# Performance work log

Hardware: AMD Instinct MI355X
Metric: run time of the kernel (lower is better)

The kernel has to match this reference:

```python
import jax, jax.numpy as jnp
import numpy as np

C = 1024      # BIGNET_DIM
GROUPS = 256  # (1024*1024) / group_size(4096)

def _dequant(q4, norm):
    # q4: [GROUPS, 2048] ints in [0,256) packing two 4-bit codes per byte
    # (even positions = low nibble, odd positions = high nibble, as in
    #  block_quantize_4bit / block_dequantize_4bit). norm: [GROUPS, 1].
    lo = q4 % 16
    hi = q4 // 16
    q8 = jnp.stack([lo, hi], axis=-1).reshape(GROUPS, -1).astype(jnp.float32)  # [GROUPS, 4096]
    w = (q8 / 15.0 * 2.0 - 1.0) * norm
    return w.reshape(C, C)  # [out_features, in_features]

def setup_inputs() -> dict:
    key = jax.random.key(0)
    ks = jax.random.split(key, 6)
    x = jax.random.normal(ks[0], (16384, C), jnp.float32)
    wq4 = jax.random.randint(ks[1], (18, GROUPS, 2048), 0, 256, jnp.int32)
    wnorm = jax.random.uniform(ks[2], (18, GROUPS, 1), dtype=jnp.float32) * 0.05 + 1e-3
    lora_a = jax.random.normal(ks[3], (3, 32, C), jnp.float32) * 0.02
    lora_b = jax.random.normal(ks[4], (3, C, 32), jnp.float32) * 0.01
    ln_gamma = jnp.ones((5, C), jnp.float32)
    ln_beta = jnp.zeros((5, C), jnp.float32)
    return {"x": x, "wq4": wq4, "wnorm": wnorm, "lora_a": lora_a,
            "lora_b": lora_b, "ln_gamma": ln_gamma, "ln_beta": ln_beta}

def reference(x, wq4, wnorm, lora_a, lora_b, ln_gamma, ln_beta):
    def lin(h, i):
        # dequantize group-wise int4 weight, then linear (bias=False)
        return h @ _dequant(wq4[i], wnorm[i]).T

    def block(h, b, li):
        y = lin(h, 3 * b)
        if li is not None:  # QLoRALinear: parallel fp32 low-rank path
            y = y + (h @ lora_a[li].T) @ lora_b[li].T
        y = jax.nn.relu(y)
        y = jax.nn.relu(lin(y, 3 * b + 1))
        y = lin(y, 3 * b + 2)
        return y + h  # residual

    def ln(h, i):
        mu = jnp.mean(h, axis=-1, keepdims=True)
        var = jnp.mean((h - mu) ** 2, axis=-1, keepdims=True)
        return (h - mu) * jax.lax.rsqrt(var + 1e-5) * ln_gamma[i] + ln_beta[i]

    h = block(x, 0, 0); h = ln(h, 0)
    h = block(h, 1, None); h = ln(h, 1)
    h = block(h, 2, 1); h = ln(h, 2)
    h = block(h, 3, None); h = ln(h, 3)
    h = block(h, 4, 2); h = ln(h, 4)
    h = block(h, 5, None)
    return h
```

## Files before the change

kernel.cpp:

```cpp
#include <hip/hip_runtime.h>

typedef __bf16 bf16x8 __attribute__((ext_vector_type(8)));
typedef float f32x4 __attribute__((ext_vector_type(4)));

__device__ __forceinline__ unsigned short f32_to_bf16u(float f) {
  unsigned int u = __float_as_uint(f);
  u += 0x7fffu + ((u >> 16) & 1u);
  return (unsigned short)(u >> 16);
}
__device__ __forceinline__ float bf16u_to_f32(unsigned short s) {
  return __uint_as_float((unsigned int)s << 16);
}

__device__ __forceinline__ void async_copy16(const void* gptr, void* lptr) {
  __builtin_amdgcn_global_load_lds(
      (__attribute__((address_space(1))) void*)(unsigned long long)gptr,
      (__attribute__((address_space(3))) void*)(unsigned long long)lptr,
      16, 0, 0);
}

__global__ __launch_bounds__(256) void lora_ba_kernel(
    const float* __restrict__ lora_a, const float* __restrict__ lora_b,
    float* __restrict__ Wba)
{
  const int bid = blockIdx.x;
  const int li = bid >> 10;
  const int o = bid & 1023;
  const float* B = lora_b + li * 32768 + o * 32;
  const float* A = lora_a + li * 32768;
  const int c = threadIdx.x * 4;
  float4 acc = {0.f, 0.f, 0.f, 0.f};
#pragma unroll
  for (int r = 0; r < 32; r++) {
    const float br = B[r];
    const float4 a = *(const float4*)&A[r * 1024 + c];
    acc.x += br * a.x; acc.y += br * a.y; acc.z += br * a.z; acc.w += br * a.w;
  }
  *(float4*)&Wba[((size_t)li << 20) + o * 1024 + c] = acc;
}

__global__ __launch_bounds__(256) void dequant_kernel(
    const int* __restrict__ wq4, const float* __restrict__ wnorm,
    const float* __restrict__ Wba, unsigned short* __restrict__ Wd)
{
  const int gi = blockIdx.x * 256 + threadIdx.x;
  const int w = gi >> 19;
  const int rem = gi & 524287;
  const int q = wq4[gi];
  const float norm = wnorm[(w << 8) + (rem >> 11)];
  float w0 = ((float)(q & 15) * (2.0f / 15.0f) - 1.0f) * norm;
  float w1 = ((float)(q >> 4) * (2.0f / 15.0f) - 1.0f) * norm;
  const int p = rem << 1;
  const int li = (w == 0) ? 0 : (w == 6) ? 1 : (w == 12) ? 2 : -1;
  if (li >= 0) {
    const float2 ba = *(const float2*)&Wba[((size_t)li << 20) + p];
    w0 += ba.x;
    w1 += ba.y;
  }
  const unsigned int packed =
      ((unsigned int)f32_to_bf16u(w1) << 16) | (unsigned int)f32_to_bf16u(w0);
  *(unsigned int*)&Wd[((size_t)w << 20) + p] = packed;
}

__global__ __launch_bounds__(256) void cast_bf16_kernel(
    const float* __restrict__ x, unsigned short* __restrict__ o)
{
  const int i = blockIdx.x * 256 + threadIdx.x;
  const float4 v = ((const float4*)x)[i];
  ushort4 b;
  b.x = f32_to_bf16u(v.x);
  b.y = f32_to_bf16u(v.y);
  b.z = f32_to_bf16u(v.z);
  b.w = f32_to_bf16u(v.w);
  ((ushort4*)o)[i] = b;
}

template <int EPIL>
__global__ __launch_bounds__(512, 2) void gemm_bt(
    const unsigned short* __restrict__ A, const unsigned short* __restrict__ W,
    void* __restrict__ Out, const unsigned short* __restrict__ Res)
{
  constexpr int K = 1024;
  constexpr int N = 1024;
  __shared__ unsigned short lds[2][4][8192];

  const int tid = threadIdx.x;
  const int lane = tid & 63;
  const int wv = tid >> 6;
  const int wm = wv >> 2;
  const int wn = wv & 3;

  const int bid = blockIdx.x;
  const int l = (bid & 7) * 32 + (bid >> 3);
  const int m0 = (l >> 2) << 8;
  const int n0 = (l & 3) << 8;

  const int fr = lane & 15;
  const int q = lane >> 4;
  const int fr7 = fr & 7;

  const int srow = tid >> 3;
  const int schk = (tid & 7) ^ (srow & 7);
  const unsigned short* Asrc = A + (size_t)(m0 + srow) * K + schk * 8;
  const int nb0 = ((srow >> 5) << 6) + (srow & 31);
  const unsigned short* Wsrc = W + (size_t)(n0 + nb0) * K + schk * 8;

#define STAGE_A(mq, dbuf, kt)                                          \
  do {                                                                 \
    const unsigned short* s_ = Asrc + (size_t)(mq) * 64 * K + (kt);    \
    unsigned short* d_ = &lds[dbuf][(mq) ? 2 : 0][tid * 8];            \
    async_copy16(s_, d_);                                              \
    async_copy16(s_ + (size_t)128 * K, d_ + 4096);                     \
  } while (0)
#define STAGE_B(nq, dbuf, kt)                                          \
  do {                                                                 \
    const unsigned short* s_ = Wsrc + (size_t)(nq) * 32 * K + (kt);    \
    unsigned short* d_ = &lds[dbuf][(nq) ? 3 : 1][tid * 8];            \
    async_copy16(s_, d_);                                              \
    async_copy16(s_ + (size_t)128 * K, d_ + 4096);                     \
  } while (0)

  const int a_lane = (wm * 64 + fr) * 64;
  const int b_lane = (wn * 32 + fr) * 64;
  const int c0 = (q ^ fr7) << 3;
  const int c1 = ((4 + q) ^ fr7) << 3;

#define LDA4(dbuf, mq)                                                               \
  do {                                                                               \
    _Pragma("unroll") for (int ri = 0; ri < 4; ++ri) {                               \
      af[ri][0] = *(const bf16x8*)&lds[dbuf][(mq) ? 2 : 0][a_lane + ri * 1024 + c0]; \
      af[ri][1] = *(const bf16x8*)&lds[dbuf][(mq) ? 2 : 0][a_lane + ri * 1024 + c1]; \
    }                                                                                \
  } while (0)
#define LDB2(dst, dbuf, nq)                                                          \
  do {                                                                               \
    _Pragma("unroll") for (int rj = 0; rj < 2; ++rj) {                               \
      dst[rj][0] = *(const bf16x8*)&lds[dbuf][(nq) ? 3 : 1][b_lane + rj * 1024 + c0];\
      dst[rj][1] = *(const bf16x8*)&lds[dbuf][(nq) ? 3 : 1][b_lane + rj * 1024 + c1];\
    }                                                                                \
  } while (0)

#define MFMA16(ib, jb, BB)                                                    \
  do {                                                                        \
    _Pragma("unroll") for (int i2 = 0; i2 < 4; ++i2)                          \
    _Pragma("unroll") for (int j2 = 0; j2 < 2; ++j2) {                        \
      acc[(ib) + i2][(jb) + j2] = __builtin_amdgcn_mfma_f32_16x16x32_bf16(    \
          af[i2][0], BB[j2][0], acc[(ib) + i2][(jb) + j2], 0, 0, 0);          \
      acc[(ib) + i2][(jb) + j2] = __builtin_amdgcn_mfma_f32_16x16x32_bf16(    \
          af[i2][1], BB[j2][1], acc[(ib) + i2][(jb) + j2], 0, 0, 0);          \
    }                                                                         \
  } while (0)

#define PHASE_MFMA(ib, jb, BB)                           \
  do {                                                   \
    __builtin_amdgcn_s_barrier();                        \
    asm volatile("s_waitcnt lgkmcnt(0)" ::: "memory");   \
    __builtin_amdgcn_s_setprio(1);                       \
    MFMA16(ib, jb, BB);                                  \
    __builtin_amdgcn_s_setprio(0);                       \
    __builtin_amdgcn_s_barrier();                        \
  } while (0)
#define PHASE_MFMA_VM(ib, jb, BB)                        \
  do {                                                   \
    __builtin_amdgcn_s_barrier();                        \
    asm volatile("s_waitcnt lgkmcnt(0)" ::: "memory");   \
    __builtin_amdgcn_s_setprio(1);                       \
    MFMA16(ib, jb, BB);                                  \
    __builtin_amdgcn_s_setprio(0);                       \
    asm volatile("s_waitcnt vmcnt(6)" ::: "memory");     \
    __builtin_amdgcn_s_barrier();                        \
  } while (0)

  f32x4 acc[8][4];
#pragma unroll
  for (int a_ = 0; a_ < 8; ++a_)
#pragma unroll
    for (int b_ = 0; b_ < 4; ++b_) acc[a_][b_] = (f32x4){0.f, 0.f, 0.f, 0.f};

  bf16x8 af[4][2], bf0[2][2], bf1[2][2];

  STAGE_A(0, 0, 0);
  STAGE_B(0, 0, 0);
  STAGE_A(1, 0, 0);
  STAGE_B(1, 0, 0);
  STAGE_A(0, 1, 64);
  STAGE_B(0, 1, 64);
  STAGE_A(1, 1, 64);
  asm volatile("s_waitcnt vmcnt(6)" ::: "memory");
  __builtin_amdgcn_s_barrier();

  for (int it = 0; it < K / 128; ++it) {
    const int kb = it * 128;
    const int k2 = (kb + 128 < K) ? (kb + 128) : (K - 64);
    const int k3 = (kb + 192 < K) ? (kb + 192) : (K - 64);

    LDA4(0, 0);
    LDB2(bf0, 0, 0);
    STAGE_B(1, 1, kb + 64);
    PHASE_MFMA(0, 0, bf0);
    LDB2(bf1, 0, 1);
    STAGE_A(0, 0, k2);
    PHASE_MFMA(0, 2, bf1);
    LDA4(0, 1);
    STAGE_B(0, 0, k2);
    PHASE_MFMA(4, 0, bf0);
    STAGE_A(1, 0, k2);
    PHASE_MFMA_VM(4, 2, bf1);
    LDA4(1, 0);
    LDB2(bf0, 1, 0);
    STAGE_B(1, 0, k2);
    PHASE_MFMA(0, 0, bf0);
    LDB2(bf1, 1, 1);
    STAGE_A(0, 1, k3);
    PHASE_MFMA(0, 2, bf1);
    LDA4(1, 1);
    STAGE_B(0, 1, k3);
    PHASE_MFMA(4, 0, bf0);
    STAGE_A(1, 1, k3);
    PHASE_MFMA_VM(4, 2, bf1);
  }

  const int mb = m0 + wm * 128 + q * 4;
  const int nb = n0 + wn * 64 + fr;
#pragma unroll
  for (int i2 = 0; i2 < 8; ++i2) {
#pragma unroll
    for (int r = 0; r < 4; ++r) {
      const int m = mb + i2 * 16 + r;
#pragma unroll
      for (int j2 = 0; j2 < 4; ++j2) {
        const int n = nb + j2 * 16;
        float v = acc[i2][j2][r];
        if (EPIL == 0) {
          v = v > 0.f ? v : 0.f;
          ((unsigned short*)Out)[(size_t)m * N + n] = f32_to_bf16u(v);
        } else if (EPIL == 1) {
          v += bf16u_to_f32(Res[(size_t)m * N + n]);
          ((unsigned short*)Out)[(size_t)m * N + n] = f32_to_bf16u(v);
        } else {
          v += bf16u_to_f32(Res[(size_t)m * N + n]);
          ((float*)Out)[(size_t)m * N + n] = v;
        }
      }
    }
  }
#undef STAGE_A
#undef STAGE_B
#undef LDA4
#undef LDB2
#undef MFMA16
#undef PHASE_MFMA
#undef PHASE_MFMA_VM
}

__global__ __launch_bounds__(256) void ln_kernel(
    const unsigned short* __restrict__ s_bf, const float* __restrict__ gamma,
    const float* __restrict__ beta, unsigned short* __restrict__ h_bf)
{
  const int row = blockIdx.x;
  const int tid = threadIdx.x;
  const size_t base = (size_t)row * 1024;
  const ushort4 u = ((const ushort4*)(s_bf + base))[tid];
  float v0 = bf16u_to_f32(u.x), v1 = bf16u_to_f32(u.y);
  float v2 = bf16u_to_f32(u.z), v3 = bf16u_to_f32(u.w);
  float s = v0 + v1 + v2 + v3;
  float s2 = v0 * v0 + v1 * v1 + v2 * v2 + v3 * v3;
#pragma unroll
  for (int off = 32; off > 0; off >>= 1) {
    s += __shfl_down(s, off, 64);
    s2 += __shfl_down(s2, off, 64);
  }
  __shared__ float red[8];
  if ((tid & 63) == 0) {
    red[tid >> 6] = s;
    red[4 + (tid >> 6)] = s2;
  }
  __syncthreads();
  s = red[0] + red[1] + red[2] + red[3];
  s2 = red[4] + red[5] + red[6] + red[7];
  const float mu = s * (1.0f / 1024.0f);
  const float var = s2 * (1.0f / 1024.0f) - mu * mu;
  const float rs = rsqrtf(var + 1e-5f);
  const float4 g = ((const float4*)gamma)[tid];
  const float4 bb = ((const float4*)beta)[tid];
  ushort4 ob;
  ob.x = f32_to_bf16u((v0 - mu) * rs * g.x + bb.x);
  ob.y = f32_to_bf16u((v1 - mu) * rs * g.y + bb.y);
  ob.z = f32_to_bf16u((v2 - mu) * rs * g.z + bb.z);
  ob.w = f32_to_bf16u((v3 - mu) * rs * g.w + bb.w);
  ((ushort4*)(h_bf + base))[tid] = ob;
}

extern "C" void kernel_launch(void* const* d_in, const int* in_sizes, int n_in,
                              void* d_out, int out_size, void* d_ws, size_t ws_size,
                              hipStream_t stream)
{
  const float* x = (const float*)d_in[0];
  const int* wq4 = (const int*)d_in[1];
  const float* wnorm = (const float*)d_in[2];
  const float* lora_a = (const float*)d_in[3];
  const float* lora_b = (const float*)d_in[4];
  const float* ln_g = (const float*)d_in[5];
  const float* ln_b = (const float*)d_in[6];
  float* out = (float*)d_out;

  char* ws = (char*)d_ws;
  unsigned short* Wd   = (unsigned short*)(ws);
  unsigned short* x_bf = (unsigned short*)(ws + 37748736);
  unsigned short* t1   = (unsigned short*)(ws + 71303168);
  unsigned short* t2   = (unsigned short*)(ws + 104857600);
  unsigned short* s_bf = (unsigned short*)(ws + 138412032);
  unsigned short* h_bf = (unsigned short*)(ws + 171966464);
  float* Wba           = (float*)(ws + 138412032);

  lora_ba_kernel<<<3072, 256, 0, stream>>>(lora_a, lora_b, Wba);
  dequant_kernel<<<36864, 256, 0, stream>>>(wq4, wnorm, Wba, Wd);
  cast_bf16_kernel<<<16384, 256, 0, stream>>>(x, x_bf);

  const unsigned short* hb = x_bf;
  const unsigned short* hres = x_bf;
  for (int b = 0; b < 6; b++) {
    const unsigned short* W0 = Wd + (size_t)(3 * b + 0) * 1048576;
    const unsigned short* W1 = Wd + (size_t)(3 * b + 1) * 1048576;
    const unsigned short* W2 = Wd + (size_t)(3 * b + 2) * 1048576;
    gemm_bt<0><<<256, 512, 0, stream>>>(hb, W0, t1, nullptr);
    gemm_bt<0><<<256, 512, 0, stream>>>(t1, W1, t2, nullptr);
    if (b < 5) {
      gemm_bt<1><<<256, 512, 0, stream>>>(t2, W2, s_bf, hres);
      ln_kernel<<<16384, 256, 0, stream>>>(s_bf, ln_g + b * 1024, ln_b + b * 1024, h_bf);
      hb = h_bf;
      hres = h_bf;
    } else {
      gemm_bt<2><<<256, 512, 0, stream>>>(t2, W2, out, hres);
    }
  }
  (void)in_sizes; (void)n_in; (void)out_size; (void)ws_size;
}
```

Measured before the change: 875.1 us.

## Software-pipeline LDS fragment loads under MFMA phases in the GEMM main loop

Restructures the GEMM main loop so the LDS fragment reads for the next phase are issued inside the current MFMA phase, before its closing barrier, rather than after it. The first fragments are prefetched before the loop. The explicit lgkmcnt(0) wait at each phase start is removed, leaving the compiler to insert waits, and the vmcnt threshold is relaxed from 6 to 4 and moved earlier. The goal is to hide LDS read latency behind MFMA work. The risks are higher register pressure and an incorrect read/write ordering on LDS buffers if the barrier placement is off.

```diff
diff --git a/kernel.cpp b/kernel.cpp
--- a/kernel.cpp
+++ b/kernel.cpp
@@ -142,6 +142,7 @@
 
 #define MFMA16(ib, jb, BB)                                                    \
   do {                                                                        \
+    __builtin_amdgcn_s_setprio(1);                                            \
     _Pragma("unroll") for (int i2 = 0; i2 < 4; ++i2)                          \
     _Pragma("unroll") for (int j2 = 0; j2 < 2; ++j2) {                        \
       acc[(ib) + i2][(jb) + j2] = __builtin_amdgcn_mfma_f32_16x16x32_bf16(    \
@@ -149,27 +150,11 @@
       acc[(ib) + i2][(jb) + j2] = __builtin_amdgcn_mfma_f32_16x16x32_bf16(    \
           af[i2][1], BB[j2][1], acc[(ib) + i2][(jb) + j2], 0, 0, 0);          \
     }                                                                         \
-  } while (0)
-
-#define PHASE_MFMA(ib, jb, BB)                           \
-  do {                                                   \
-    __builtin_amdgcn_s_barrier();                        \
-    asm volatile("s_waitcnt lgkmcnt(0)" ::: "memory");   \
-    __builtin_amdgcn_s_setprio(1);                       \
-    MFMA16(ib, jb, BB);                                  \
-    __builtin_amdgcn_s_setprio(0);                       \
-    __builtin_amdgcn_s_barrier();                        \
-  } while (0)
-#define PHASE_MFMA_VM(ib, jb, BB)                        \
-  do {                                                   \
-    __builtin_amdgcn_s_barrier();                        \
-    asm volatile("s_waitcnt lgkmcnt(0)" ::: "memory");   \
-    __builtin_amdgcn_s_setprio(1);                       \
-    MFMA16(ib, jb, BB);                                  \
-    __builtin_amdgcn_s_setprio(0);                       \
-    asm volatile("s_waitcnt vmcnt(6)" ::: "memory");     \
-    __builtin_amdgcn_s_barrier();                        \
-  } while (0)
+    __builtin_amdgcn_s_setprio(0);                                            \
+  } while (0)
+
+#define OPEN_BAR  __builtin_amdgcn_s_barrier()
+#define CLOSE_BAR asm volatile("s_barrier" ::: "memory")
 
   f32x4 acc[8][4];
 #pragma unroll
@@ -188,36 +173,56 @@
   STAGE_A(1, 1, 64);
   asm volatile("s_waitcnt vmcnt(6)" ::: "memory");
   __builtin_amdgcn_s_barrier();
+  LDA4(0, 0);
+  LDB2(bf0, 0, 0);
 
   for (int it = 0; it < K / 128; ++it) {
     const int kb = it * 128;
     const int k2 = (kb + 128 < K) ? (kb + 128) : (K - 64);
     const int k3 = (kb + 192 < K) ? (kb + 192) : (K - 64);
 
+    LDB2(bf1, 0, 1);
+    STAGE_B(1, 1, kb + 64);
+    OPEN_BAR;
+    MFMA16(0, 0, bf0);
+    CLOSE_BAR;
+    STAGE_A(0, 0, k2);
+    OPEN_BAR;
+    MFMA16(0, 2, bf1);
+    LDA4(0, 1);
+    CLOSE_BAR;
+    STAGE_B(0, 0, k2);
+    OPEN_BAR;
+    MFMA16(4, 0, bf0);
+    asm volatile("s_waitcnt vmcnt(4)" ::: "memory");
+    CLOSE_BAR;
+    LDB2(bf0, 1, 0);
+    STAGE_A(1, 0, k2);
+    OPEN_BAR;
+    MFMA16(4, 2, bf1);
+    LDA4(1, 0);
+    CLOSE_BAR;
+    LDB2(bf1, 1, 1);
+    STAGE_B(1, 0, k2);
+    OPEN_BAR;
+    MFMA16(0, 0, bf0);
+    CLOSE_BAR;
+    STAGE_A(0, 1, k3);
+    OPEN_BAR;
+    MFMA16(0, 2, bf1);
+    LDA4(1, 1);
+    CLOSE_BAR;
+    STAGE_B(0, 1, k3);
+    OPEN_BAR;
+    MFMA16(4, 0, bf0);
+    asm volatile("s_waitcnt vmcnt(4)" ::: "memory");
+    CLOSE_BAR;
+    LDB2(bf0, 0, 0);
+    STAGE_A(1, 1, k3);
+    OPEN_BAR;
+    MFMA16(4, 2, bf1);
     LDA4(0, 0);
-    LDB2(bf0, 0, 0);
-    STAGE_B(1, 1, kb + 64);
-    PHASE_MFMA(0, 0, bf0);
-    LDB2(bf1, 0, 1);
-    STAGE_A(0, 0, k2);
-    PHASE_MFMA(0, 2, bf1);
-    LDA4(0, 1);
-    STAGE_B(0, 0, k2);
-    PHASE_MFMA(4, 0, bf0);
-    STAGE_A(1, 0, k2);
-    PHASE_MFMA_VM(4, 2, bf1);
-    LDA4(1, 0);
-    LDB2(bf0, 1, 0);
-    STAGE_B(1, 0, k2);
-    PHASE_MFMA(0, 0, bf0);
-    LDB2(bf1, 1, 1);
-    STAGE_A(0, 1, k3);
-    PHASE_MFMA(0, 2, bf1);
-    LDA4(1, 1);
-    STAGE_B(0, 1, k3);
-    PHASE_MFMA(4, 0, bf0);
-    STAGE_A(1, 1, k3);
-    PHASE_MFMA_VM(4, 2, bf1);
+    CLOSE_BAR;
   }
 
   const int mb = m0 + wm * 128 + q * 4;
@@ -249,8 +254,8 @@
 #undef LDA4
 #undef LDB2
 #undef MFMA16
-#undef PHASE_MFMA
-#undef PHASE_MFMA_VM
+#undef OPEN_BAR
+#undef CLOSE_BAR
 }
 
 __global__ __launch_bounds__(256) void ln_kernel(
```

Measured after the change: 934.7 us. 1.07x slower.

## Merge GEMM MFMA phases into two larger barrier windows per half-iteration

Applied to the files above, without the earlier changes.

Restructures the GEMM main loop so each half-iteration runs one combined MFMA window over both B fragments, replacing two separate phases. This halves the number of barrier pairs and reorders the async global-to-LDS stage copies and LDS fragment loads around the new windows. The prologue and in-loop staging order is changed to match. The aim is less barrier overhead and longer uninterrupted MFMA runs. The cost is more outstanding LDS loads and registers per window, and the vmcnt-based waits must still line up with the changed stage order.

```diff
diff --git a/kernel.cpp b/kernel.cpp
--- a/kernel.cpp
+++ b/kernel.cpp
@@ -151,21 +151,23 @@
     }                                                                         \
   } while (0)
 
-#define PHASE_MFMA(ib, jb, BB)                           \
+#define WINDOW(ib)                                       \
   do {                                                   \
     __builtin_amdgcn_s_barrier();                        \
     asm volatile("s_waitcnt lgkmcnt(0)" ::: "memory");   \
     __builtin_amdgcn_s_setprio(1);                       \
-    MFMA16(ib, jb, BB);                                  \
+    MFMA16(ib, 0, bf0);                                  \
+    MFMA16(ib, 2, bf1);                                  \
     __builtin_amdgcn_s_setprio(0);                       \
     __builtin_amdgcn_s_barrier();                        \
   } while (0)
-#define PHASE_MFMA_VM(ib, jb, BB)                        \
+#define WINDOW_VM(ib)                                    \
   do {                                                   \
     __builtin_amdgcn_s_barrier();                        \
     asm volatile("s_waitcnt lgkmcnt(0)" ::: "memory");   \
     __builtin_amdgcn_s_setprio(1);                       \
-    MFMA16(ib, jb, BB);                                  \
+    MFMA16(ib, 0, bf0);                                  \
+    MFMA16(ib, 2, bf1);                                  \
     __builtin_amdgcn_s_setprio(0);                       \
     asm volatile("s_waitcnt vmcnt(6)" ::: "memory");     \
     __builtin_amdgcn_s_barrier();                        \
@@ -185,7 +187,7 @@
   STAGE_B(1, 0, 0);
   STAGE_A(0, 1, 64);
   STAGE_B(0, 1, 64);
-  STAGE_A(1, 1, 64);
+  STAGE_B(1, 1, 64);
   asm volatile("s_waitcnt vmcnt(6)" ::: "memory");
   __builtin_amdgcn_s_barrier();
 
@@ -196,28 +198,24 @@
 
     LDA4(0, 0);
     LDB2(bf0, 0, 0);
-    STAGE_B(1, 1, kb + 64);
-    PHASE_MFMA(0, 0, bf0);
     LDB2(bf1, 0, 1);
+    STAGE_A(1, 1, kb + 64);
+    WINDOW(0);
+    LDA4(0, 1);
     STAGE_A(0, 0, k2);
-    PHASE_MFMA(0, 2, bf1);
-    LDA4(0, 1);
     STAGE_B(0, 0, k2);
-    PHASE_MFMA(4, 0, bf0);
-    STAGE_A(1, 0, k2);
-    PHASE_MFMA_VM(4, 2, bf1);
+    STAGE_B(1, 0, k2);
+    WINDOW_VM(4);
     LDA4(1, 0);
     LDB2(bf0, 1, 0);
-    STAGE_B(1, 0, k2);
-    PHASE_MFMA(0, 0, bf0);
     LDB2(bf1, 1, 1);
+    STAGE_A(1, 0, k2);
+    WINDOW(0);
+    LDA4(1, 1);
     STAGE_A(0, 1, k3);
-    PHASE_MFMA(0, 2, bf1);
-    LDA4(1, 1);
     STAGE_B(0, 1, k3);
-    PHASE_MFMA(4, 0, bf0);
-    STAGE_A(1, 1, k3);
-    PHASE_MFMA_VM(4, 2, bf1);
+    STAGE_B(1, 1, k3);
+    WINDOW_VM(4);
   }
 
   const int mb = m0 + wm * 128 + q * 4;
@@ -249,8 +247,8 @@
 #undef LDA4
 #undef LDB2
 #undef MFMA16
-#undef PHASE_MFMA
-#undef PHASE_MFMA_VM
+#undef WINDOW
+#undef WINDOW_VM
 }
 
 __global__ __launch_bounds__(256) void ln_kernel(
```

New measurement: 936.2 us. 1.07x slower.

## Double-buffer A fragments and prefetch LDS reads one phase ahead in GEMM loop

Applied to the files above, without the earlier changes.

Restructures the GEMM main loop so LDS-to-register fragment loads for the next MFMA phase are issued before the current phase's MFMAs. Two A-fragment register sets are kept, and partial lgkmcnt waits plus sched_barrier replace the full lgkmcnt(0) waits. This is meant to hide LDS read latency behind matrix-core work. It costs extra VGPRs for the second A fragment set, and the hand-counted wait thresholds must match the number of outstanding LDS operations to stay correct.

```diff
diff --git a/kernel.cpp b/kernel.cpp
--- a/kernel.cpp
+++ b/kernel.cpp
@@ -125,11 +125,11 @@
   const int c0 = (q ^ fr7) << 3;
   const int c1 = ((4 + q) ^ fr7) << 3;
 
-#define LDA4(dbuf, mq)                                                               \
+#define LDA4(dst, dbuf, mq)                                                          \
   do {                                                                               \
     _Pragma("unroll") for (int ri = 0; ri < 4; ++ri) {                               \
-      af[ri][0] = *(const bf16x8*)&lds[dbuf][(mq) ? 2 : 0][a_lane + ri * 1024 + c0]; \
-      af[ri][1] = *(const bf16x8*)&lds[dbuf][(mq) ? 2 : 0][a_lane + ri * 1024 + c1]; \
+      dst[ri][0] = *(const bf16x8*)&lds[dbuf][(mq) ? 2 : 0][a_lane + ri * 1024 + c0];\
+      dst[ri][1] = *(const bf16x8*)&lds[dbuf][(mq) ? 2 : 0][a_lane + ri * 1024 + c1];\
     }                                                                                \
   } while (0)
 #define LDB2(dst, dbuf, nq)                                                          \
@@ -140,36 +140,23 @@
     }                                                                                \
   } while (0)
 
-#define MFMA16(ib, jb, BB)                                                    \
+#define MFMA16(ib, jb, AF, BB)                                                \
   do {                                                                        \
     _Pragma("unroll") for (int i2 = 0; i2 < 4; ++i2)                          \
     _Pragma("unroll") for (int j2 = 0; j2 < 2; ++j2) {                        \
       acc[(ib) + i2][(jb) + j2] = __builtin_amdgcn_mfma_f32_16x16x32_bf16(    \
-          af[i2][0], BB[j2][0], acc[(ib) + i2][(jb) + j2], 0, 0, 0);          \
+          AF[i2][0], BB[j2][0], acc[(ib) + i2][(jb) + j2], 0, 0, 0);          \
       acc[(ib) + i2][(jb) + j2] = __builtin_amdgcn_mfma_f32_16x16x32_bf16(    \
-          af[i2][1], BB[j2][1], acc[(ib) + i2][(jb) + j2], 0, 0, 0);          \
+          AF[i2][1], BB[j2][1], acc[(ib) + i2][(jb) + j2], 0, 0, 0);          \
     }                                                                         \
   } while (0)
 
-#define PHASE_MFMA(ib, jb, BB)                           \
-  do {                                                   \
-    __builtin_amdgcn_s_barrier();                        \
-    asm volatile("s_waitcnt lgkmcnt(0)" ::: "memory");   \
-    __builtin_amdgcn_s_setprio(1);                       \
-    MFMA16(ib, jb, BB);                                  \
-    __builtin_amdgcn_s_setprio(0);                       \
-    __builtin_amdgcn_s_barrier();                        \
-  } while (0)
-#define PHASE_MFMA_VM(ib, jb, BB)                        \
-  do {                                                   \
-    __builtin_amdgcn_s_barrier();                        \
-    asm volatile("s_waitcnt lgkmcnt(0)" ::: "memory");   \
-    __builtin_amdgcn_s_setprio(1);                       \
-    MFMA16(ib, jb, BB);                                  \
-    __builtin_amdgcn_s_setprio(0);                       \
-    asm volatile("s_waitcnt vmcnt(6)" ::: "memory");     \
-    __builtin_amdgcn_s_barrier();                        \
-  } while (0)
+#define BARx asm volatile("s_barrier" ::: "memory")
+#define WAITL(n) asm volatile("s_waitcnt lgkmcnt(" #n ")" ::: "memory")
+#define VM6 asm volatile("s_waitcnt vmcnt(6)" ::: "memory")
+#define SCHEDB __builtin_amdgcn_sched_barrier(0)
+#define PRIO1 __builtin_amdgcn_s_setprio(1)
+#define PRIO0 __builtin_amdgcn_s_setprio(0)
 
   f32x4 acc[8][4];
 #pragma unroll
@@ -177,7 +164,7 @@
 #pragma unroll
     for (int b_ = 0; b_ < 4; ++b_) acc[a_][b_] = (f32x4){0.f, 0.f, 0.f, 0.f};
 
-  bf16x8 af[4][2], bf0[2][2], bf1[2][2];
+  bf16x8 afA[4][2], afB[4][2], bf0[2][2], bf1[2][2];
 
   STAGE_A(0, 0, 0);
   STAGE_B(0, 0, 0);
@@ -187,37 +174,57 @@
   STAGE_B(0, 1, 64);
   STAGE_A(1, 1, 64);
   asm volatile("s_waitcnt vmcnt(6)" ::: "memory");
-  __builtin_amdgcn_s_barrier();
+  BARx;
+  LDA4(afA, 0, 0);
+  LDB2(bf0, 0, 0);
 
   for (int it = 0; it < K / 128; ++it) {
     const int kb = it * 128;
     const int k2 = (kb + 128 < K) ? (kb + 128) : (K - 64);
     const int k3 = (kb + 192 < K) ? (kb + 192) : (K - 64);
 
-    LDA4(0, 0);
+    LDB2(bf1, 0, 1);
+    STAGE_B(1, 1, kb + 64);
+    BARx; WAITL(4); SCHEDB;
+    PRIO1; MFMA16(0, 0, afA, bf0); PRIO0;
+    BARx;
+    LDA4(afB, 0, 1);
+    STAGE_A(0, 0, k2);
+    BARx; WAITL(8); SCHEDB;
+    PRIO1; MFMA16(0, 2, afA, bf1); PRIO0;
+    BARx;
+    STAGE_B(0, 0, k2);
+    BARx; WAITL(0); SCHEDB;
+    PRIO1; MFMA16(4, 0, afB, bf0); PRIO0;
+    BARx;
+    LDA4(afA, 1, 0);
+    LDB2(bf0, 1, 0);
+    STAGE_A(1, 0, k2);
+    BARx; WAITL(12); SCHEDB;
+    PRIO1; MFMA16(4, 2, afB, bf1); PRIO0;
+    VM6;
+    BARx;
+    LDB2(bf1, 1, 1);
+    STAGE_B(1, 0, k2);
+    BARx; WAITL(4); SCHEDB;
+    PRIO1; MFMA16(0, 0, afA, bf0); PRIO0;
+    BARx;
+    LDA4(afB, 1, 1);
+    STAGE_A(0, 1, k3);
+    BARx; WAITL(8); SCHEDB;
+    PRIO1; MFMA16(0, 2, afA, bf1); PRIO0;
+    BARx;
+    STAGE_B(0, 1, k3);
+    BARx; WAITL(0); SCHEDB;
+    PRIO1; MFMA16(4, 0, afB, bf0); PRIO0;
+    BARx;
+    LDA4(afA, 0, 0);
     LDB2(bf0, 0, 0);
-    STAGE_B(1, 1, kb + 64);
-    PHASE_MFMA(0, 0, bf0);
-    LDB2(bf1, 0, 1);
-    STAGE_A(0, 0, k2);
-    PHASE_MFMA(0, 2, bf1);
-    LDA4(0, 1);
-    STAGE_B(0, 0, k2);
-    PHASE_MFMA(4, 0, bf0);
-    STAGE_A(1, 0, k2);
-    PHASE_MFMA_VM(4, 2, bf1);
-    LDA4(1, 0);
-    LDB2(bf0, 1, 0);
-    STAGE_B(1, 0, k2);
-    PHASE_MFMA(0, 0, bf0);
-    LDB2(bf1, 1, 1);
-    STAGE_A(0, 1, k3);
-    PHASE_MFMA(0, 2, bf1);
-    LDA4(1, 1);
-    STAGE_B(0, 1, k3);
-    PHASE_MFMA(4, 0, bf0);
     STAGE_A(1, 1, k3);
-    PHASE_MFMA_VM(4, 2, bf1);
+    BARx; WAITL(12); SCHEDB;
+    PRIO1; MFMA16(4, 2, afB, bf1); PRIO0;
+    VM6;
+    BARx;
   }
 
   const int mb = m0 + wm * 128 + q * 4;
@@ -249,8 +256,12 @@
 #undef LDA4
 #undef LDB2
 #undef MFMA16
-#undef PHASE_MFMA
-#undef PHASE_MFMA_VM
+#undef BARx
+#undef WAITL
+#undef VM6
+#undef SCHEDB
+#undef PRIO1
+#undef PRIO0
 }
 
 __global__ __launch_bounds__(256) void ln_kernel(
```

After: 1.175 ms. +34.3%, slower.
